# Performance work log

Hardware: AMD Instinct MI355X
Metric: run time of the kernel (lower is better)

Reference implementation:

```python
import jax, jax.numpy as jnp
import numpy as np

L_IN, L_FREQ, L_OUT = 128, 64, 64
C_IN, C_OUT, T_DIM = 64, 64, 256
SPIN = 1

# ---------- self-contained spin-weighted SHT (MW sampling), replacing s2fft ----------

def _mw_thetas(L, extended):
    n = 2 * L - 1 if extended else L
    return (2 * np.arange(n) + 1) * np.pi / (2 * L - 1)

def _wigner_d_stack(L, thetas, n):
    # d^l_{m,n}(theta) = <l,m| exp(-i theta Jy) |l,n>, computed via eigh of the
    # Hermitian angular-momentum operator Jy. Output (ntheta, L, 2L-1), m at col L-1+m.
    nth = len(thetas)
    out = np.zeros((nth, L, 2 * L - 1), dtype=np.float64)
    for l in range(abs(n), L):
        dim = 2 * l + 1
        m = np.arange(-l, l).astype(np.float64)
        ap = np.sqrt(l * (l + 1.0) - m * (m + 1.0))
        Jy = np.zeros((dim, dim), dtype=np.complex128)
        i = np.arange(dim - 1)
        Jy[i + 1, i] = -0.5j * ap
        Jy[i, i + 1] = 0.5j * ap
        lam, V = np.linalg.eigh(Jy)
        coeff = V * np.conj(V[l + n, :])[None, :]
        phases = np.exp(-1j * np.outer(lam, thetas))
        out[:, l, L - 1 - l:L + l] = (coeff @ phases).T.real
    return out

def _mw_quad_weights(L):
    # per-theta weights on the mirror-extended grid: q_t = (1/(2L-1)) sum_k w(k) e^{ik theta_t}
    # with w(k) = int_0^pi e^{ik t} sin(t) dt
    k = np.arange(-(L - 1), L)
    den = np.where(np.abs(k) == 1, 1, 1 - k * k).astype(np.float64)
    w = np.where(k % 2 == 0, 2.0 / den, 0.0).astype(np.complex128)
    w[k == 1] = 0.5j * np.pi
    w[k == -1] = -0.5j * np.pi
    th = _mw_thetas(L, True)
    return ((w[None, :] * np.exp(1j * np.outer(th, k))).sum(1) / (2 * L - 1)).real

# transform kernels are constants (built once at import, numpy)
_D_FWD = jnp.asarray(_wigner_d_stack(L_IN, _mw_thetas(L_IN, True), -SPIN) * _mw_quad_weights(L_IN)[:, None, None], jnp.float32)
_D_INV = jnp.asarray(_wigner_d_stack(L_OUT, _mw_thetas(L_OUT, False), -SPIN), jnp.float32)
_CL_IN = jnp.asarray(((-1.0) ** SPIN) * np.sqrt((2 * np.arange(L_IN) + 1) / (4 * np.pi)), jnp.float32)
_CL_OUT = jnp.asarray(((-1.0) ** SPIN) * np.sqrt((2 * np.arange(L_OUT) + 1) / (4 * np.pi)), jnp.float32)
_m_all = np.arange(-(L_IN - 1), L_IN)
_PARITY = jnp.asarray(np.where((_m_all + SPIN) % 2 == 0, 1.0, -1.0), jnp.float32)

def sht_forward(x):
    # x: (L_IN, 2*L_IN-1, C) real spatial -> flm: (L_IN, 2*L_IN-1, C) complex, m at L_IN-1+m
    nphi = 2 * L_IN - 1
    ftm = jnp.fft.fftshift(jnp.fft.fft(x, axis=1), axes=1) * (2 * jnp.pi / nphi)
    # mirror extension in theta with (-1)^(m+spin) parity (all channels at once)
    g_ext = jnp.concatenate([ftm, _PARITY[None, :, None] * ftm[::-1][1:]], axis=0)
    flm = jnp.einsum('tlm,tmc->lmc', _D_FWD, g_ext)
    return flm * _CL_IN[:, None, None]

def sht_inverse(flm):
    # flm: (L_OUT, 2*L_OUT-1, C) complex -> (L_OUT, 2*L_OUT-1, C) real spatial
    ftm = jnp.einsum('tlm,lmc->tmc', _D_INV, flm * _CL_OUT[:, None, None])
    return (jnp.fft.ifft(jnp.fft.ifftshift(ftm, axes=1), axis=1) * (2 * L_OUT - 1)).real

def resize_flm(flm, l_in, l_out):
    # centered truncation / zero-pad of (L, 2L-1, C) harmonic coefficients
    if l_out <= l_in:
        d = l_in - l_out
        return flm[:l_out, d:d + 2 * l_out - 1]
    d = l_out - l_in
    return jnp.pad(flm, ((0, d), (d, d), (0, 0)))

# ---------- inputs and parameters ----------

def setup_inputs():
    key = jax.random.key(0)
    ks = jax.random.split(key, 12)
    n = lambda i, shape, s: jax.random.normal(ks[i], shape, jnp.float32) * s
    return {
        'x': jax.random.normal(ks[0], (L_IN, 2 * L_IN - 1, C_IN), jnp.float32),
        't_emb': jax.random.normal(ks[1], (T_DIM,), jnp.float32),
        'spec_conv_w': n(2, (C_IN, C_OUT), (1.0 / C_IN) ** 0.5),
        'spec_conv_b': jnp.zeros((C_OUT,), jnp.float32),
        'spec_wr': n(3, (L_FREQ, C_IN, C_OUT), (0.5 / C_IN) ** 0.5),
        'spec_wi': n(4, (L_FREQ, C_IN, C_OUT), (0.5 / C_IN) ** 0.5),
        'spec_tr_w': n(5, (T_DIM, L_FREQ), (1.0 / T_DIM) ** 0.5),
        'spec_tr_b': jnp.zeros((L_FREQ,), jnp.float32),
        'spec_ti_w': n(6, (T_DIM, L_FREQ), (1.0 / T_DIM) ** 0.5),
        'spec_ti_b': jnp.zeros((L_FREQ,), jnp.float32),
        'spat_conv1_w': n(7, (C_IN, C_OUT), (1.0 / C_IN) ** 0.5),
        'spat_conv1_b': jnp.zeros((C_OUT,), jnp.float32),
        'spat_t_w': n(8, (T_DIM, 2 * C_OUT), (1.0 / T_DIM) ** 0.5),
        'spat_t_b': jnp.zeros((2 * C_OUT,), jnp.float32),
        'spat_weight': n(9, (C_OUT, C_OUT), 0.01),
        'spat_conv2_w': n(10, (C_OUT, C_OUT), (1.0 / C_OUT) ** 0.5),
        'spat_conv2_b': jnp.zeros((C_OUT,), jnp.float32),
        'ln_scale': jnp.ones((C_OUT,), jnp.float32),
        'ln_bias': jnp.zeros((C_OUT,), jnp.float32),
    }

def reference(x, t_emb, spec_conv_w, spec_conv_b, spec_wr, spec_wi, spec_tr_w, spec_tr_b, spec_ti_w, spec_ti_b, spat_conv1_w, spat_conv1_b, spat_t_w, spat_t_b, spat_weight, spat_conv2_w, spat_conv2_b, ln_scale, ln_bias):
    # ----- SphericalSpectralTimeConv branch -----
    flm = sht_forward(x)                                   # (L_IN, 2L_IN-1, C_IN) complex
    flm = resize_flm(flm, L_IN, L_FREQ)                    # (L_FREQ, 2L_FREQ-1, C_IN)
    conv_flm = jnp.einsum('lmi,io->lmo', flm, spec_conv_w) + spec_conv_b
    t_c = (t_emb @ spec_tr_w + spec_tr_b) + 1j * (t_emb @ spec_ti_w + spec_ti_b)   # (L_FREQ,)
    w = t_c[:, None, None] * (spec_wr + 1j * spec_wi)      # (L_FREQ, C_IN, C_OUT)
    flm = jnp.einsum('lmi,lio->lmo', flm, w) + conv_flm
    xs = sht_inverse(resize_flm(flm, L_FREQ, L_OUT))       # (L_OUT, 2L_OUT-1, C_OUT) real
    xs = xs / (jnp.linalg.norm(xs, axis=-1, keepdims=True) + 1e-6)
    # ----- SpatialTimeConv branch (path='down') -----
    h = jnp.einsum('lmi,io->lmo', x, spat_conv1_w) + spat_conv1_b
    t = t_emb @ spat_t_w + spat_t_b
    w_t, b_t = t[:C_OUT], t[C_OUT:]
    h = jnp.einsum('lmi,io->lmo', h, w_t[None, :] * spat_weight)
    h = sht_inverse(resize_flm(sht_forward(h), L_IN, L_OUT))
    h = jnp.einsum('lmi,io->lmo', h, spat_conv2_w) + spat_conv2_b + b_t
    # ----- combine: add, gelu, LayerNorm (eps=1e-6 over channels) -----
    y = jax.nn.gelu(xs + h)
    mu = jnp.mean(y, axis=-1, keepdims=True)
    var = jnp.var(y, axis=-1, keepdims=True)
    return (y - mu) * jax.lax.rsqrt(var + 1e-6) * ln_scale + ln_bias
```

## Files before the change

kernel.cpp:

```cpp
#include <hip/hip_runtime.h>
#include <math.h>

#define DPI 3.141592653589793238462643383279502884

__device__ float g_Deff[1040384];
__device__ float g_Dinv[520192];
__device__ int g_wig_done = 0;

__device__ __forceinline__ float wave_sum64(float v) {
#pragma unroll
  for (int off = 32; off > 0; off >>= 1) v += __shfl_xor(v, off, 64);
  return v;
}

__device__ __forceinline__ float gelu_tanh(float v) {
  float u = 0.7978845608028654f * (v + 0.044715f * v * v * v);
  return 0.5f * v * (1.0f + tanhf(u));
}

#define CN255F ((float)(-2.0 * DPI / 255.0))
#define CN127F ((float)(2.0 * DPI / 127.0))


__device__ __forceinline__ void dft_block(int idx, int tid, const float* __restrict__ x,
                                          float* __restrict__ Are, float* __restrict__ Aim,
                                          float* __restrict__ Bre, float* __restrict__ Bim,
                                          char* sm) {
  float* xs_ = (float*)sm;
  int t = idx >> 2, ph = (idx >> 1) & 1, mh = idx & 1;
  float* ore = ph ? Bre : Are;
  float* oim = ph ? Bim : Aim;
  int pbase = ph * 128;
  int Ktot = ph ? 127 : 128;
  int cg_ = tid & 15, mg = tid >> 4;
  float wr[2], wi[2], rc[2], rs[2];
#pragma unroll
  for (int j = 0; j < 2; ++j) {
    int m = mh * 32 + mg * 2 + j;
    __sincosf(CN255F * (float)m, &rs[j], &rc[j]);
    int r0 = (m * pbase) % 255;
    __sincosf(CN255F * (float)r0, &wi[j], &wr[j]);
  }
  float accr[2][4], acci[2][4];
#pragma unroll
  for (int j = 0; j < 2; ++j)
#pragma unroll
    for (int q = 0; q < 4; ++q) { accr[j][q] = 0.f; acci[j][q] = 0.f; }
  for (int k0 = 0; k0 < Ktot; k0 += 64) {
    int kn = (Ktot - k0 < 64) ? Ktot - k0 : 64;
    __syncthreads();
    {
      const float4* src = (const float4*)(x + ((size_t)t * 255 + pbase + k0) * 64);
      float4* dst = (float4*)xs_;
      int lim = kn * 16;
#pragma unroll
      for (int q = 0; q < 4; ++q) {
        int fidx = tid + q * 256;
        if (fidx < lim) dst[fidx] = src[fidx];
      }
    }
    __syncthreads();
#pragma unroll 2
    for (int k = 0; k < kn; ++k) {
      float4 xv = *(const float4*)&xs_[k * 64 + cg_ * 4];
      float xv4[4] = {xv.x, xv.y, xv.z, xv.w};
#pragma unroll
      for (int j = 0; j < 2; ++j) {
#pragma unroll
        for (int q = 0; q < 4; ++q) {
          accr[j][q] = fmaf(xv4[q], wr[j], accr[j][q]);
          acci[j][q] = fmaf(xv4[q], wi[j], acci[j][q]);
        }
        float nw = wr[j] * rc[j] - wi[j] * rs[j];
        wi[j] = fmaf(wr[j], rs[j], wi[j] * rc[j]);
        wr[j] = nw;
      }
    }
  }
#pragma unroll
  for (int j = 0; j < 2; ++j) {
    int mi = mh * 32 + mg * 2 + j;
    size_t ob = ((size_t)t * 64 + mi) * 64 + cg_ * 4;
    *(float4*)(ore + ob) = make_float4(accr[j][0], accr[j][1], accr[j][2], accr[j][3]);
    *(float4*)(oim + ob) = make_float4(acci[j][0], acci[j][1], acci[j][2], acci[j][3]);
  }
}

__device__ __forceinline__ void wigner_block(int wb, int tid, char* sm) {
  if (__hip_atomic_load(&g_wig_done, __ATOMIC_RELAXED, __HIP_MEMORY_SCOPE_AGENT)) return;
  float* LF = (float*)sm;
  double* red = (double*)(sm + 512);
  float* clf = (float*)(sm + 1024);
  int mode = (wb < 128) ? 0 : 1;
  int t, mm;
  if (mode == 0) { t = wb; mm = tid; }
  else { mm = wb - 128; t = (tid < 64) ? tid : 63; }
  if (tid < 64) clf[tid] = (float)(-sqrt((2.0 * tid + 1.0) / (4.0 * DPI)));
  if (tid < 128) LF[tid] = (tid == 0) ? 0.f : logf((float)tid);
  __syncthreads();
  for (int s = 1; s < 128; s <<= 1) {
    float add = (tid < 128 && tid >= s) ? LF[tid - s] : 0.f;
    __syncthreads();
    if (tid < 128) LF[tid] += add;
    __syncthreads();
  }
  double denomN = (mode == 0) ? 255.0 : 127.0;
  double beta = (2.0 * t + 1.0) * DPI / denomN;
  float coeff = 1.0f;
  if (mode == 0) {
    if (tid < 63) {
      int k = 2 * (tid + 1);
      red[tid] = 8.0 * cos((double)k * beta) / (1.0 - (double)k * (double)k);
    } else if (tid == 63) {
      red[63] = 4.0;
    }
    __syncthreads();
    for (int s = 32; s > 0; s >>= 1) {
      if (tid < s) red[tid] += red[tid + s];
      __syncthreads();
    }
    double s = red[0] / 255.0;
    if (t == 127) s *= 0.5;
    coeff = (float)(s * (2.0 * DPI / 255.0));
  }
  bool active = (mode == 0) ? (tid < 127) : (tid < 64);
  if (!active) return;
  int m = mm - 63;
  double chd, shd;
  sincos(0.5 * beta, &shd, &chd);
  float cbf = (float)cos(beta);
  float chf = (float)chd, shf = (float)shd;
  int am = (m < 0) ? -m : m;
  int l0v = (am > 1) ? am : 1;
  float seed;
  if (m == 0) {
    seed = -1.4142135623730951f * shf * chf;
  } else {
    int j = am;
    float lch = logf(chf), lsh = logf(shf);
    float e0 = 0.5f * (LF[2 * j] - LF[j - 1] - LF[j + 1]);
    float expo = (m >= 1) ? e0 + (float)(j - 1) * lch + (float)(j + 1) * lsh
                          : e0 + (float)(j + 1) * lch + (float)(j - 1) * lsh;
    float sv = __expf(expo);
    seed = (m >= 1 && ((m + 1) & 1)) ? -sv : sv;
  }
  float dl = seed, dm1 = 0.0f, S_cur = 0.0f;
  float mf = (float)m;
  for (int l = 0; l < 64; ++l) {
    float val = 0.0f;
    if (l >= l0v) {
      val = dl * coeff * clf[l];
      float Ld = (float)l, lp = Ld + 1.0f;
      float S_next = sqrtf((lp * lp - mf * mf) * (lp * lp - 1.0f));
      float num1 = (2.0f * Ld + 1.0f) * (Ld * lp * cbf + mf);
      float dn = (num1 * dl - lp * S_cur * dm1) / (Ld * S_next);
      dm1 = dl; dl = dn; S_cur = S_next;
    }
    if (mode == 0) g_Deff[((size_t)t * 127 + mm) * 64 + l] = val;
    else g_Dinv[((size_t)mm * 64 + l) * 64 + t] = val;
  }
}

__device__ __forceinline__ void a2_block(int l, int tid, const float* __restrict__ temb,
                                         const float* __restrict__ trw, const float* __restrict__ trb,
                                         const float* __restrict__ tiw, const float* __restrict__ tib,
                                         const float* __restrict__ scw, const float* __restrict__ swr,
                                         const float* __restrict__ swi, float2* __restrict__ A2,
                                         char* sm) {
  float* fb1 = (float*)sm;
  float* fb2 = (float*)(sm + 1024);
  fb1[tid] = temb[tid] * trw[tid * 64 + l];
  fb2[tid] = temb[tid] * tiw[tid * 64 + l];
  __syncthreads();
  for (int s = 128; s > 0; s >>= 1) {
    if (tid < s) { fb1[tid] += fb1[tid + s]; fb2[tid] += fb2[tid + s]; }
    __syncthreads();
  }
  float tr = fb1[0] + trb[l], ti = fb2[0] + tib[l];
  int o = tid & 63, iq = tid >> 6;
  for (int i = iq * 16; i < iq * 16 + 16; ++i) {
    int idx = (l * 64 + i) * 64 + o;
    float r = swr[idx], s2 = swi[idx];
    A2[idx] = make_float2(scw[i * 64 + o] + tr * r - ti * s2, tr * s2 + ti * r);
  }
}

__device__ __forceinline__ void m_block(int j, int tid, const float* __restrict__ temb,
                                        const float* __restrict__ stw, const float* __restrict__ stb,
                                        const float* __restrict__ c1w, const float* __restrict__ c1b,
                                        const float* __restrict__ sweight, float* __restrict__ Mm,
                                        float* __restrict__ bias2, char* sm) {
  float* fb1 = (float*)sm;
  float* fb2 = (float*)(sm + 1024);
  int o = tid & 63, part = tid >> 6;
  float p = 0.f;
  for (int k = part * 64; k < part * 64 + 64; ++k)
    p = fmaf(temb[k], stw[k * 128 + o], p);
  fb1[part * 64 + o] = p;
  __syncthreads();
  if (part == 0) fb2[o] = fb1[o] + fb1[64 + o] + fb1[128 + o] + fb1[192 + o] + stb[o];
  __syncthreads();
  float tvo = fb2[o];
  float q = 0.f;
  for (int i = part * 16; i < part * 16 + 16; ++i)
    q = fmaf(c1w[j * 64 + i], sweight[i * 64 + o], q);
  __syncthreads();
  fb1[part * 64 + o] = q;
  __syncthreads();
  if (part == 0) Mm[j * 64 + o] = tvo * (fb1[o] + fb1[64 + o] + fb1[128 + o] + fb1[192 + o]);
  if (j == 0) {
    float bq = 0.f;
    for (int i = part * 16; i < part * 16 + 16; ++i)
      bq = fmaf(c1b[i], sweight[i * 64 + o], bq);
    __syncthreads();
    fb1[part * 64 + o] = bq;
    __syncthreads();
    if (part == 0) bias2[o] = tvo * (fb1[o] + fb1[64 + o] + fb1[128 + o] + fb1[192 + o]);
  }
}

__device__ __forceinline__ void tv_block(int tid, const float* __restrict__ temb,
                                         const float* __restrict__ stw, const float* __restrict__ stb,
                                         float* __restrict__ tv, char* sm) {
  float* fb1 = (float*)sm;
  int o = tid & 127, part = tid >> 7;
  float p = 0.f;
  for (int k = part * 128; k < part * 128 + 128; ++k)
    p = fmaf(temb[k], stw[k * 128 + o], p);
  fb1[part * 128 + o] = p;
  __syncthreads();
  if (part == 0) tv[o] = fb1[o] + fb1[128 + o] + stb[o];
}

__global__ __launch_bounds__(256, 2) void ct_pre(
    const float* __restrict__ x, const float* __restrict__ temb,
    const float* __restrict__ trw, const float* __restrict__ trb,
    const float* __restrict__ tiw, const float* __restrict__ tib,
    const float* __restrict__ stw, const float* __restrict__ stb,
    const float* __restrict__ scw, const float* __restrict__ swr,
    const float* __restrict__ swi, const float* __restrict__ c1w,
    const float* __restrict__ c1b, const float* __restrict__ sweight,
    float2* __restrict__ A2, float* __restrict__ Mm,
    float* __restrict__ bias2, float* __restrict__ tv,
    float* __restrict__ ftmA_re, float* __restrict__ ftmA_im,
    float* __restrict__ ftmB_re, float* __restrict__ ftmB_im) {
  __shared__ __align__(16) char sm[16384];
  int vb = blockIdx.x;
  int tid = threadIdx.x;
  if (vb < 255) wigner_block(vb, tid, sm);
  else if (vb < 319) a2_block(vb - 255, tid, temb, trw, trb, tiw, tib, scw, swr, swi, A2, sm);
  else if (vb < 383) m_block(vb - 319, tid, temb, stw, stb, c1w, c1b, sweight, Mm, bias2, sm);
  else if (vb < 384) tv_block(tid, temb, stw, stb, tv, sm);
  else dft_block(vb - 384, tid, x, ftmA_re, ftmA_im, ftmB_re, ftmB_im, sm);
}

__global__ __launch_bounds__(256) void ct_projf(const float* __restrict__ fAre,
                                                const float* __restrict__ fAim,
                                                const float* __restrict__ fBre,
                                                const float* __restrict__ fBim,
                                                float* __restrict__ flmA_re, float* __restrict__ flmA_im,
                                                float* __restrict__ flmB_re, float* __restrict__ flmB_im) {
  __shared__ float Dsh[64][32];
  __shared__ float fr_[64][64], fi_[64][64];
  int mm = blockIdx.x, lh = blockIdx.y, th = blockIdx.z;
  float* ore = th ? flmB_re : flmA_re;
  float* oim = th ? flmB_im : flmA_im;
  int tb = th * 64;
  int mi = (mm >= 63) ? (mm - 63) : (63 - mm);
  float csign = (mm >= 63) ? 1.0f : -1.0f;
  int tid = threadIdx.x;
  int cg_ = tid & 15, lg = tid >> 4;
  for (int e = tid; e < 64 * 32; e += 256) {
    int r = e >> 5, li = e & 31;
    Dsh[r][li] = g_Deff[((size_t)(tb + r) * 127 + mm) * 64 + lh * 32 + li];
  }
  for (int e = tid; e < 64 * 64; e += 256) {
    int r = e >> 6, c = e & 63;
    size_t idx = ((size_t)(tb + r) * 64 + mi) * 64 + c;
    fr_[r][c] = fAre[idx] + fBre[idx];
    fi_[r][c] = csign * (fAim[idx] + fBim[idx]);
  }
  __syncthreads();
  float ar[2][4], ai[2][4];
#pragma unroll
  for (int li = 0; li < 2; ++li)
#pragma unroll
    for (int q = 0; q < 4; ++q) { ar[li][q] = 0.f; ai[li][q] = 0.f; }
#pragma unroll 4
  for (int k = 0; k < 64; ++k) {
    float4 fr4 = *(const float4*)&fr_[k][cg_ * 4];
    float4 fi4 = *(const float4*)&fi_[k][cg_ * 4];
    float2 d2 = *(const float2*)&Dsh[k][lg * 2];
    float frv[4] = {fr4.x, fr4.y, fr4.z, fr4.w};
    float fiv[4] = {fi4.x, fi4.y, fi4.z, fi4.w};
    float dv[2] = {d2.x, d2.y};
#pragma unroll
    for (int li = 0; li < 2; ++li)
#pragma unroll
      for (int q = 0; q < 4; ++q) {
        ar[li][q] = fmaf(dv[li], frv[q], ar[li][q]);
        ai[li][q] = fmaf(dv[li], fiv[q], ai[li][q]);
      }
  }
#pragma unroll
  for (int li = 0; li < 2; ++li) {
    size_t row = ((size_t)mm * 64 + lh * 32 + lg * 2 + li) * 64 + cg_ * 4;
    *(float4*)(ore + row) = make_float4(ar[li][0], ar[li][1], ar[li][2], ar[li][3]);
    *(float4*)(oim + row) = make_float4(ai[li][0], ai[li][1], ai[li][2], ai[li][3]);
  }
}

__global__ __launch_bounds__(256) void ct_mix(const float* __restrict__ flmA_re,
                                              const float* __restrict__ flmA_im,
                                              const float* __restrict__ flmB_re,
                                              const float* __restrict__ flmB_im,
                                              const float2* __restrict__ A2,
                                              const float* __restrict__ Mm,
                                              const float* __restrict__ scb,
                                              const float* __restrict__ bias2,
                                              float* __restrict__ s_re, float* __restrict__ s_im,
                                              float* __restrict__ h_re, float* __restrict__ h_im) {
  __shared__ float Ar_[64][32], Ai_[64][32], Msh[64][32];
  __shared__ float Br_[64][65], Bi_[64][65];
  __shared__ float rb[256];
  int l = blockIdx.x, mh = blockIdx.y, oh = blockIdx.z;
  int tid = threadIdx.x;
  int og = tid & 15, mg = tid >> 4;
  rb[tid] = (mh == 0 && tid < 128) ? g_Deff[((size_t)tid * 127 + 63) * 64 + l] : 0.f;
  __syncthreads();
  for (int s = 128; s > 0; s >>= 1) {
    if (tid < s) rb[tid] += rb[tid + s];
    __syncthreads();
  }
  float slv = rb[0];
  for (int e = tid; e < 64 * 32; e += 256) {
    int r = e >> 5, oi = e & 31;
    float2 aa = A2[((size_t)l * 64 + r) * 64 + oh * 32 + oi];
    Ar_[r][oi] = aa.x; Ai_[r][oi] = aa.y;
    Msh[r][oi] = Mm[r * 64 + oh * 32 + oi];
  }
  for (int e = tid; e < 64 * 64; e += 256) {
    int mi = e >> 6, i = e & 63;
    int gmm = mh * 64 + mi; if (gmm > 126) gmm = 126;
    size_t idx = ((size_t)gmm * 64 + l) * 64 + i;
    Br_[mi][i] = flmA_re[idx] + flmB_re[idx];
    Bi_[mi][i] = flmA_im[idx] + flmB_im[idx];
  }
  __syncthreads();
  int o0 = oh * 32 + og * 2;
  float b0[2] = {scb[o0], scb[o0 + 1]};
  float sr[4][2], si[4][2], hr[4][2], hi[4][2];
#pragma unroll
  for (int jm = 0; jm < 4; ++jm)
#pragma unroll
    for (int qo = 0; qo < 2; ++qo) {
      sr[jm][qo] = b0[qo]; si[jm][qo] = 0.f; hr[jm][qo] = 0.f; hi[jm][qo] = 0.f;
    }
#pragma unroll 4
  for (int k = 0; k < 64; ++k) {
    float2 ar2 = *(const float2*)&Ar_[k][og * 2];
    float2 ai2 = *(const float2*)&Ai_[k][og * 2];
    float2 mv2 = *(const float2*)&Msh[k][og * 2];
    float br4[4], bi4[4];
#pragma unroll
    for (int jm = 0; jm < 4; ++jm) {
      br4[jm] = Br_[mg * 4 + jm][k];
      bi4[jm] = Bi_[mg * 4 + jm][k];
    }
    float arv[2] = {ar2.x, ar2.y}, aiv[2] = {ai2.x, ai2.y}, mvv[2] = {mv2.x, mv2.y};
#pragma unroll
    for (int jm = 0; jm < 4; ++jm)
#pragma unroll
      for (int qo = 0; qo < 2; ++qo) {
        sr[jm][qo] = fmaf(br4[jm], arv[qo], sr[jm][qo]);
        sr[jm][qo] = fmaf(-bi4[jm], aiv[qo], sr[jm][qo]);
        si[jm][qo] = fmaf(br4[jm], aiv[qo], si[jm][qo]);
        si[jm][qo] = fmaf(bi4[jm], arv[qo], si[jm][qo]);
        hr[jm][qo] = fmaf(br4[jm], mvv[qo], hr[jm][qo]);
        hi[jm][qo] = fmaf(bi4[jm], mvv[qo], hi[jm][qo]);
      }
  }
  float bb[2] = {bias2[o0], bias2[o0 + 1]};
#pragma unroll
  for (int jm = 0; jm < 4; ++jm) {
    int gmm = mh * 64 + mg * 4 + jm;
    if (gmm > 126) continue;
    if (gmm == 63) {
#pragma unroll
      for (int qo = 0; qo < 2; ++qo)
        hr[jm][qo] = fmaf(255.0f * slv, bb[qo], hr[jm][qo]);
    }
    size_t row = ((size_t)gmm * 64 + l) * 64 + o0;
    *(float2*)(s_re + row) = make_float2(sr[jm][0], sr[jm][1]);
    *(float2*)(s_im + row) = make_float2(si[jm][0], si[jm][1]);
    *(float2*)(h_re + row) = make_float2(hr[jm][0], hr[jm][1]);
    *(float2*)(h_im + row) = make_float2(hi[jm][0], hi[jm][1]);
  }
}

__global__ __launch_bounds__(256) void ct_proji(const float* __restrict__ s_re,
                                                const float* __restrict__ s_im,
                                                const float* __restrict__ h_re,
                                                const float* __restrict__ h_im,
                                                float* __restrict__ fos_re, float* __restrict__ fos_im,
                                                float* __restrict__ foh_re, float* __restrict__ foh_im) {
  __shared__ float Dsh[64][64];
  __shared__ float Br_[64][32], Bi_[64][32];
  int mm = blockIdx.x, br = blockIdx.y, ch = blockIdx.z;
  const float* ire = br ? h_re : s_re;
  const float* iim = br ? h_im : s_im;
  float* ore = br ? foh_re : fos_re;
  float* oim = br ? foh_im : fos_im;
  int tid = threadIdx.x;
  int cg_ = tid & 15, tg = tid >> 4;
  for (int e = tid; e < 64 * 64; e += 256) {
    int r = e >> 6, tt = e & 63;
    Dsh[r][tt] = g_Dinv[((size_t)mm * 64 + r) * 64 + tt];
  }
  for (int e = tid; e < 64 * 32; e += 256) {
    int r = e >> 5, cc = e & 31;
    size_t idx = ((size_t)mm * 64 + r) * 64 + ch * 32 + cc;
    Br_[r][cc] = ire[idx];
    Bi_[r][cc] = iim[idx];
  }
  __syncthreads();
  float ar[4][2], ai[4][2];
#pragma unroll
  for (int j = 0; j < 4; ++j)
#pragma unroll
    for (int q = 0; q < 2; ++q) { ar[j][q] = 0.f; ai[j][q] = 0.f; }
#pragma unroll 4
  for (int k = 0; k < 64; ++k) {
    float4 d4 = *(const float4*)&Dsh[k][tg * 4];
    float2 fr2 = *(const float2*)&Br_[k][cg_ * 2];
    float2 fi2 = *(const float2*)&Bi_[k][cg_ * 2];
    float dv[4] = {d4.x, d4.y, d4.z, d4.w};
    float frv[2] = {fr2.x, fr2.y}, fiv[2] = {fi2.x, fi2.y};
#pragma unroll
    for (int j = 0; j < 4; ++j)
#pragma unroll
      for (int q = 0; q < 2; ++q) {
        ar[j][q] = fmaf(dv[j], frv[q], ar[j][q]);
        ai[j][q] = fmaf(dv[j], fiv[q], ai[j][q]);
      }
  }
#pragma unroll
  for (int j = 0; j < 4; ++j) {
    int t = tg * 4 + j;
    size_t ob = ((size_t)t * 127 + mm) * 64 + ch * 32 + cg_ * 2;
    *(float2*)(ore + ob) = make_float2(ar[j][0], ar[j][1]);
    *(float2*)(oim + ob) = make_float2(ai[j][0], ai[j][1]);
  }
}

__global__ __launch_bounds__(256) void ct_idft(const float* __restrict__ fos_re,
                                               const float* __restrict__ fos_im,
                                               const float* __restrict__ foh_re,
                                               const float* __restrict__ foh_im,
                                               float* __restrict__ xsbA, float* __restrict__ xsbB,
                                               float* __restrict__ hsbA, float* __restrict__ hsbB) {
  __shared__ float Br_[32][64], Bi_[32][64];
  int t = blockIdx.x, br = blockIdx.y;
  int z = blockIdx.z;
  int ph = z >> 1, kh = z & 1;
  const float* fre = br ? foh_re : fos_re;
  const float* fim = br ? foh_im : fos_im;
  float* outp = br ? (kh ? hsbB : hsbA) : (kh ? xsbB : xsbA);
  int kbase = kh * 64;
  int Ktot = kh ? 63 : 64;
  int tid = threadIdx.x;
  int cg_ = tid & 15, pg = tid >> 4;
  float wc[4], ws[4], rc[4], rs[4];
#pragma unroll
  for (int j = 0; j < 4; ++j) {
    int gp = ph * 64 + pg * 4 + j; if (gp > 126) gp = 126;
    __sincosf(CN127F * (float)gp, &rs[j], &rc[j]);
    int r0 = ((kbase - 63) * gp) % 127;
    __sincosf(CN127F * (float)r0, &ws[j], &wc[j]);
  }
  float acc[4][4];
#pragma unroll
  for (int j = 0; j < 4; ++j)
#pragma unroll
    for (int q = 0; q < 4; ++q) acc[j][q] = 0.f;
  for (int k0 = 0; k0 < Ktot; k0 += 32) {
    int kn = (Ktot - k0 < 32) ? Ktot - k0 : 32;
    __syncthreads();
    for (int e = tid; e < 32 * 64; e += 256) {
      int r = e >> 6, j = e & 63;
      if (r < kn) {
        size_t bidx = ((size_t)t * 127 + kbase + k0 + r) * 64 + j;
        Br_[r][j] = fre[bidx]; Bi_[r][j] = fim[bidx];
      }
    }
    __syncthreads();
#pragma unroll 2
    for (int k = 0; k < kn; ++k) {
      float4 b_r = *(const float4*)&Br_[k][cg_ * 4];
      float4 b_i = *(const float4*)&Bi_[k][cg_ * 4];
      float brv[4] = {b_r.x, b_r.y, b_r.z, b_r.w};
      float biv[4] = {b_i.x, b_i.y, b_i.z, b_i.w};
#pragma unroll
      for (int j = 0; j < 4; ++j) {
#pragma unroll
        for (int q = 0; q < 4; ++q) {
          acc[j][q] = fmaf(brv[q], wc[j], acc[j][q]);
          acc[j][q] = fmaf(biv[q], -ws[j], acc[j][q]);
        }
        float nw = wc[j] * rc[j] - ws[j] * rs[j];
        ws[j] = fmaf(wc[j], rs[j], ws[j] * rc[j]);
        wc[j] = nw;
      }
    }
  }
#pragma unroll
  for (int j = 0; j < 4; ++j) {
    int gp = ph * 64 + pg * 4 + j;
    if (gp > 126) continue;
    *(float4*)(outp + ((size_t)t * 127 + gp) * 64 + cg_ * 4) =
        make_float4(acc[j][0], acc[j][1], acc[j][2], acc[j][3]);
  }
}

__global__ __launch_bounds__(256) void ct_fin(const float* __restrict__ xsbA,
                                              const float* __restrict__ xsbB,
                                              const float* __restrict__ hsbA,
                                              const float* __restrict__ hsbB,
                                              const float* __restrict__ c2w,
                                              const float* __restrict__ c2b,
                                              const float* __restrict__ tv,
                                              const float* __restrict__ lns,
                                              const float* __restrict__ lnb,
                                              float* __restrict__ out) {
  int w = threadIdx.x >> 6, lane = threadIdx.x & 63;
  size_t row = (size_t)blockIdx.x * 4 + w;
  size_t base = row * 64 + lane;
  float hv = hsbA[base] + hsbB[base];
  float xv = xsbA[base] + xsbB[base];
  float acc = c2b[lane] + tv[64 + lane];
#pragma unroll 16
  for (int i = 0; i < 64; ++i)
    acc = fmaf(__shfl(hv, i, 64), c2w[i * 64 + lane], acc);
  float ss = wave_sum64(xv * xv);
  xv = xv / (sqrtf(ss) + 1e-6f);
  float y = xv + acc;
  float g = gelu_tanh(y);
  float mu = wave_sum64(g) * (1.0f / 64.0f);
  float d = g - mu;
  float var = wave_sum64(d * d) * (1.0f / 64.0f);
  out[base] = d * rsqrtf(var + 1e-6f) * lns[lane] + lnb[lane];
  if (blockIdx.x == 0 && threadIdx.x == 0)
    __hip_atomic_store(&g_wig_done, 1, __ATOMIC_RELAXED, __HIP_MEMORY_SCOPE_AGENT);
}

extern "C" void kernel_launch(void* const* d_in, const int* in_sizes, int n_in,
                              void* d_out, int out_size, void* d_ws, size_t ws_size,
                              hipStream_t stream) {
  const float* x = (const float*)d_in[0];
  const float* temb = (const float*)d_in[1];
  const float* scw = (const float*)d_in[2];
  const float* scb = (const float*)d_in[3];
  const float* swr = (const float*)d_in[4];
  const float* swi = (const float*)d_in[5];
  const float* strw = (const float*)d_in[6];
  const float* strb = (const float*)d_in[7];
  const float* stiw = (const float*)d_in[8];
  const float* stib = (const float*)d_in[9];
  const float* c1w = (const float*)d_in[10];
  const float* c1b = (const float*)d_in[11];
  const float* stw = (const float*)d_in[12];
  const float* stb = (const float*)d_in[13];
  const float* sweight = (const float*)d_in[14];
  const float* c2w = (const float*)d_in[15];
  const float* c2b = (const float*)d_in[16];
  const float* lns = (const float*)d_in[17];
  const float* lnb = (const float*)d_in[18];
  float* out = (float*)d_out;

  char* base = (char*)d_ws;
  size_t off = 0;
  auto alloc = [&](size_t bytes) -> void* {
    void* p = base + off;
    off += (bytes + 255) & ~(size_t)255;
    return p;
  };
  float* tv = (float*)alloc(128 * sizeof(float));
  float* Mm = (float*)alloc(4096 * sizeof(float));
  float* bias2 = (float*)alloc(64 * sizeof(float));
  float2* A2 = (float2*)alloc(262144 * sizeof(float2));
  float* fosbuf = (float*)alloc(1040384 * sizeof(float));
  float* ftmA_re = (float*)alloc(524288 * sizeof(float));
  float* ftmA_im = (float*)alloc(524288 * sizeof(float));
  float* ftmB_re = (float*)alloc(524288 * sizeof(float));
  float* ftmB_im = (float*)alloc(524288 * sizeof(float));
  float* flmA_re = (float*)alloc(520192 * sizeof(float));
  float* flmA_im = (float*)alloc(520192 * sizeof(float));
  float* flmB_re = (float*)alloc(520192 * sizeof(float));
  float* flmB_im = (float*)alloc(520192 * sizeof(float));
  if (off > ws_size) return;
  float* s_re = ftmA_re;
  float* s_im = ftmA_im;
  float* h_re = ftmB_re;
  float* h_im = ftmB_im;
  float* fos_re = fosbuf;
  float* fos_im = fosbuf + 520192;
  float* foh_re = flmA_re;
  float* foh_im = flmA_im;
  float* xsbA = flmB_re;
  float* xsbB = flmB_im;
  float* hsbA = ftmA_re;
  float* hsbB = ftmA_im;

  hipLaunchKernelGGL(ct_pre, dim3(896), dim3(256), 0, stream,
                     x, temb, strw, strb, stiw, stib, stw, stb,
                     scw, swr, swi, c1w, c1b, sweight,
                     A2, Mm, bias2, tv,
                     ftmA_re, ftmA_im, ftmB_re, ftmB_im);
  hipLaunchKernelGGL(ct_projf, dim3(127, 2, 2), dim3(256), 0, stream,
                     ftmA_re, ftmA_im, ftmB_re, ftmB_im,
                     flmA_re, flmA_im, flmB_re, flmB_im);
  hipLaunchKernelGGL(ct_mix, dim3(64, 2, 2), dim3(256), 0, stream,
                     flmA_re, flmA_im, flmB_re, flmB_im, A2, Mm, scb, bias2,
                     s_re, s_im, h_re, h_im);
  hipLaunchKernelGGL(ct_proji, dim3(127, 2, 2), dim3(256), 0, stream,
                     s_re, s_im, h_re, h_im, fos_re, fos_im, foh_re, foh_im);
  hipLaunchKernelGGL(ct_idft, dim3(64, 2, 4), dim3(256), 0, stream,
                     fos_re, fos_im, foh_re, foh_im, xsbA, xsbB, hsbA, hsbB);
  hipLaunchKernelGGL(ct_fin, dim3(2032), dim3(256), 0, stream, xsbA, xsbB, hsbA, hsbB,
                     c2w, c2b, tv, lns, lnb, out);
}
```

Baseline: 194.5 us.

## Move parameter-prep blocks from ct_pre into ct_projf and merge M/tv blocks

The A2 and M/bias/tv parameter-preparation blocks move out of ct_pre and are appended as extra blocks of ct_projf, which now uses a flattened 1D grid. The 64 redundant m_block instances and the tv block are merged into a single block that stages temb, sweight and c1w in shared memory and computes tv, Mm and bias2 at once. The aim is to shorten ct_pre's critical path and to drop the recomputation of the temb projection. ct_projf's shared memory grows to 40 KB, which may lower its occupancy, and the single merged block could become a straggler.

```diff
diff --git a/kernel.cpp b/kernel.cpp
--- a/kernel.cpp
+++ b/kernel.cpp
@@ -20,7 +20,6 @@
 
 #define CN255F ((float)(-2.0 * DPI / 255.0))
 #define CN127F ((float)(2.0 * DPI / 127.0))
-
 
 __device__ __forceinline__ void dft_block(int idx, int tid, const float* __restrict__ x,
                                           float* __restrict__ Are, float* __restrict__ Aim,
@@ -178,6 +177,7 @@
   }
   float tr = fb1[0] + trb[l], ti = fb2[0] + tib[l];
   int o = tid & 63, iq = tid >> 6;
+#pragma unroll 4
   for (int i = iq * 16; i < iq * 16 + 16; ++i) {
     int idx = (l * 64 + i) * 64 + o;
     float r = swr[idx], s2 = swi[idx];
@@ -185,73 +185,64 @@
   }
 }
 
-__device__ __forceinline__ void m_block(int j, int tid, const float* __restrict__ temb,
-                                        const float* __restrict__ stw, const float* __restrict__ stb,
-                                        const float* __restrict__ c1w, const float* __restrict__ c1b,
-                                        const float* __restrict__ sweight, float* __restrict__ Mm,
-                                        float* __restrict__ bias2, char* sm) {
-  float* fb1 = (float*)sm;
-  float* fb2 = (float*)(sm + 1024);
-  int o = tid & 63, part = tid >> 6;
-  float p = 0.f;
-  for (int k = part * 64; k < part * 64 + 64; ++k)
-    p = fmaf(temb[k], stw[k * 128 + o], p);
-  fb1[part * 64 + o] = p;
-  __syncthreads();
-  if (part == 0) fb2[o] = fb1[o] + fb1[64 + o] + fb1[128 + o] + fb1[192 + o] + stb[o];
-  __syncthreads();
-  float tvo = fb2[o];
-  float q = 0.f;
-  for (int i = part * 16; i < part * 16 + 16; ++i)
-    q = fmaf(c1w[j * 64 + i], sweight[i * 64 + o], q);
-  __syncthreads();
-  fb1[part * 64 + o] = q;
-  __syncthreads();
-  if (part == 0) Mm[j * 64 + o] = tvo * (fb1[o] + fb1[64 + o] + fb1[128 + o] + fb1[192 + o]);
-  if (j == 0) {
-    float bq = 0.f;
-    for (int i = part * 16; i < part * 16 + 16; ++i)
-      bq = fmaf(c1b[i], sweight[i * 64 + o], bq);
-    __syncthreads();
-    fb1[part * 64 + o] = bq;
-    __syncthreads();
-    if (part == 0) bias2[o] = tvo * (fb1[o] + fb1[64 + o] + fb1[128 + o] + fb1[192 + o]);
-  }
-}
-
-__device__ __forceinline__ void tv_block(int tid, const float* __restrict__ temb,
-                                         const float* __restrict__ stw, const float* __restrict__ stb,
-                                         float* __restrict__ tv, char* sm) {
-  float* fb1 = (float*)sm;
-  int o = tid & 127, part = tid >> 7;
-  float p = 0.f;
-  for (int k = part * 128; k < part * 128 + 128; ++k)
-    p = fmaf(temb[k], stw[k * 128 + o], p);
-  fb1[part * 128 + o] = p;
-  __syncthreads();
-  if (part == 0) tv[o] = fb1[o] + fb1[128 + o] + stb[o];
+__device__ __forceinline__ void mstv_block(int tid, const float* __restrict__ temb,
+                                           const float* __restrict__ stw, const float* __restrict__ stb,
+                                           const float* __restrict__ c1w, const float* __restrict__ c1b,
+                                           const float* __restrict__ sweight,
+                                           float* __restrict__ tv, float* __restrict__ Mm,
+                                           float* __restrict__ bias2, char* sm) {
+  float* temb_s = (float*)sm;
+  float* swt = (float*)(sm + 1024);
+  float* c1s = (float*)(sm + 17408);
+  float* tvo_s = (float*)(sm + 34048);
+  if (tid < 64) ((float4*)temb_s)[tid] = ((const float4*)temb)[tid];
+  for (int q = tid; q < 1024; q += 256) ((float4*)swt)[q] = ((const float4*)sweight)[q];
+  for (int e = tid; e < 4096; e += 256) c1s[(e >> 6) * 65 + (e & 63)] = c1w[e];
+  __syncthreads();
+  if (tid < 128) {
+    float a0 = 0.f, a1 = 0.f, a2 = 0.f, a3 = 0.f;
+#pragma unroll 8
+    for (int k = 0; k < 256; k += 4) {
+      a0 = fmaf(temb_s[k],     stw[k * 128 + tid],       a0);
+      a1 = fmaf(temb_s[k + 1], stw[(k + 1) * 128 + tid], a1);
+      a2 = fmaf(temb_s[k + 2], stw[(k + 2) * 128 + tid], a2);
+      a3 = fmaf(temb_s[k + 3], stw[(k + 3) * 128 + tid], a3);
+    }
+    float tvv = a0 + a1 + a2 + a3 + stb[tid];
+    tv[tid] = tvv;
+    if (tid < 64) tvo_s[tid] = tvv;
+  }
+  __syncthreads();
+  {
+    int j = tid >> 2, ob = (tid & 3) * 16;
+    float acc[16];
+#pragma unroll
+    for (int q = 0; q < 16; ++q) acc[q] = 0.f;
+    for (int i = 0; i < 64; ++i) {
+      float c = c1s[j * 65 + i];
+#pragma unroll
+      for (int q = 0; q < 16; ++q) acc[q] = fmaf(c, swt[i * 64 + ob + q], acc[q]);
+    }
+#pragma unroll
+    for (int q = 0; q < 16; ++q) Mm[j * 64 + ob + q] = tvo_s[ob + q] * acc[q];
+  }
+  if (tid < 64) {
+    float acc = 0.f;
+#pragma unroll 4
+    for (int i = 0; i < 64; ++i) acc = fmaf(c1b[i], swt[i * 64 + tid], acc);
+    bias2[tid] = tvo_s[tid] * acc;
+  }
 }
 
 __global__ __launch_bounds__(256, 2) void ct_pre(
-    const float* __restrict__ x, const float* __restrict__ temb,
-    const float* __restrict__ trw, const float* __restrict__ trb,
-    const float* __restrict__ tiw, const float* __restrict__ tib,
-    const float* __restrict__ stw, const float* __restrict__ stb,
-    const float* __restrict__ scw, const float* __restrict__ swr,
-    const float* __restrict__ swi, const float* __restrict__ c1w,
-    const float* __restrict__ c1b, const float* __restrict__ sweight,
-    float2* __restrict__ A2, float* __restrict__ Mm,
-    float* __restrict__ bias2, float* __restrict__ tv,
+    const float* __restrict__ x,
     float* __restrict__ ftmA_re, float* __restrict__ ftmA_im,
     float* __restrict__ ftmB_re, float* __restrict__ ftmB_im) {
   __shared__ __align__(16) char sm[16384];
   int vb = blockIdx.x;
   int tid = threadIdx.x;
   if (vb < 255) wigner_block(vb, tid, sm);
-  else if (vb < 319) a2_block(vb - 255, tid, temb, trw, trb, tiw, tib, scw, swr, swi, A2, sm);
-  else if (vb < 383) m_block(vb - 319, tid, temb, stw, stb, c1w, c1b, sweight, Mm, bias2, sm);
-  else if (vb < 384) tv_block(tid, temb, stw, stb, tv, sm);
-  else dft_block(vb - 384, tid, x, ftmA_re, ftmA_im, ftmB_re, ftmB_im, sm);
+  else dft_block(vb - 255, tid, x, ftmA_re, ftmA_im, ftmB_re, ftmB_im, sm);
 }
 
 __global__ __launch_bounds__(256) void ct_projf(const float* __restrict__ fAre,
@@ -259,16 +250,34 @@
                                                 const float* __restrict__ fBre,
                                                 const float* __restrict__ fBim,
                                                 float* __restrict__ flmA_re, float* __restrict__ flmA_im,
-                                                float* __restrict__ flmB_re, float* __restrict__ flmB_im) {
-  __shared__ float Dsh[64][32];
-  __shared__ float fr_[64][64], fi_[64][64];
-  int mm = blockIdx.x, lh = blockIdx.y, th = blockIdx.z;
+                                                float* __restrict__ flmB_re, float* __restrict__ flmB_im,
+                                                const float* __restrict__ temb,
+                                                const float* __restrict__ trw, const float* __restrict__ trb,
+                                                const float* __restrict__ tiw, const float* __restrict__ tib,
+                                                const float* __restrict__ scw, const float* __restrict__ swr,
+                                                const float* __restrict__ swi, float2* __restrict__ A2,
+                                                const float* __restrict__ stw, const float* __restrict__ stb,
+                                                const float* __restrict__ c1w, const float* __restrict__ c1b,
+                                                const float* __restrict__ sweight,
+                                                float* __restrict__ tv, float* __restrict__ Mm,
+                                                float* __restrict__ bias2) {
+  __shared__ __align__(16) char sm[40960];
+  int tile = blockIdx.x;
+  int tid = threadIdx.x;
+  if (tile >= 508) {
+    if (tile < 572) a2_block(tile - 508, tid, temb, trw, trb, tiw, tib, scw, swr, swi, A2, sm);
+    else mstv_block(tid, temb, stw, stb, c1w, c1b, sweight, tv, Mm, bias2, sm);
+    return;
+  }
+  float (*Dsh)[32] = (float(*)[32])(sm);
+  float (*fr_)[64] = (float(*)[64])(sm + 8192);
+  float (*fi_)[64] = (float(*)[64])(sm + 24576);
+  int mm = tile >> 2, lh = (tile >> 1) & 1, th = tile & 1;
   float* ore = th ? flmB_re : flmA_re;
   float* oim = th ? flmB_im : flmA_im;
   int tb = th * 64;
   int mi = (mm >= 63) ? (mm - 63) : (63 - mm);
   float csign = (mm >= 63) ? 1.0f : -1.0f;
-  int tid = threadIdx.x;
   int cg_ = tid & 15, lg = tid >> 4;
   for (int e = tid; e < 64 * 32; e += 256) {
     int r = e >> 5, li = e & 31;
@@ -611,14 +620,13 @@
   float* hsbA = ftmA_re;
   float* hsbB = ftmA_im;
 
-  hipLaunchKernelGGL(ct_pre, dim3(896), dim3(256), 0, stream,
-                     x, temb, strw, strb, stiw, stib, stw, stb,
-                     scw, swr, swi, c1w, c1b, sweight,
-                     A2, Mm, bias2, tv,
-                     ftmA_re, ftmA_im, ftmB_re, ftmB_im);
-  hipLaunchKernelGGL(ct_projf, dim3(127, 2, 2), dim3(256), 0, stream,
+  hipLaunchKernelGGL(ct_pre, dim3(767), dim3(256), 0, stream,
+                     x, ftmA_re, ftmA_im, ftmB_re, ftmB_im);
+  hipLaunchKernelGGL(ct_projf, dim3(573), dim3(256), 0, stream,
                      ftmA_re, ftmA_im, ftmB_re, ftmB_im,
-                     flmA_re, flmA_im, flmB_re, flmB_im);
+                     flmA_re, flmA_im, flmB_re, flmB_im,
+                     temb, strw, strb, stiw, stib, scw, swr, swi, A2,
+                     stw, stb, c1w, c1b, sweight, tv, Mm, bias2);
   hipLaunchKernelGGL(ct_mix, dim3(64, 2, 2), dim3(256), 0, stream,
                      flmA_re, flmA_im, flmB_re, flmB_im, A2, Mm, scb, bias2,
                      s_re, s_im, h_re, h_im);
```

Result: faster. 179.0 us (-8.0%).
